# Performance work log

Measured on AMD Instinct MI355X. Metric: run time of the kernel, lower is better.

## Reference

```python
import jax, jax.numpy as jnp
import numpy as np

T, B, S, D = 512, 32, 512, 512
EPS = 1e-6  # LayerNorm eps


def _ln(x, g, b):
    m = jnp.mean(x, axis=-1, keepdims=True)
    v = jnp.mean((x - m) ** 2, axis=-1, keepdims=True)
    return g * (x - m) * jax.lax.rsqrt(v + EPS) + b


def setup_inputs() -> dict:
    key = jax.random.key(0)
    ks = jax.random.split(key, 10)
    sc = 1.0 / np.sqrt(D).astype(np.float32)
    return {
        "prev_layer": jax.random.normal(ks[0], (T, B, D), jnp.float32),
        "hidden": jax.random.normal(ks[1], (B, D), jnp.float32),
        "enc_output": jax.random.normal(ks[2], (B, S, D), jnp.float32),
        "memory_length": jax.random.randint(ks[3], (B,), 1, S + 1),
        # nn.Linear weights stored as [in, out] (transposed torch layout)
        "W_in": jax.random.normal(ks[4], (D, 3 * D), jnp.float32) * sc,
        "W_enc": jax.random.normal(ks[5], (D, D), jnp.float32) * sc,
        "W_attn_in": jax.random.normal(ks[6], (D, D), jnp.float32) * sc,
        "W_hidden": jax.random.normal(ks[7], (D, D), jnp.float32) * sc,
        "W_ctx": jax.random.normal(ks[8], (D, D), jnp.float32) * sc,
        # LayerNorm gains/biases (5 LNs)
        "g_pre": jnp.ones((3 * D,), jnp.float32), "b_pre": jnp.zeros((3 * D,), jnp.float32),
        "g_enc": jnp.ones((D,), jnp.float32), "b_enc": jnp.zeros((D,), jnp.float32),
        "g_attn": jnp.ones((D,), jnp.float32), "b_attn": jnp.zeros((D,), jnp.float32),
        "g_h": jnp.ones((D,), jnp.float32), "b_h": jnp.zeros((D,), jnp.float32),
        "g_c": jnp.ones((D,), jnp.float32), "b_c": jnp.zeros((D,), jnp.float32),
    }


def reference(prev_layer, hidden, enc_output, W_in, W_enc, W_attn_in, W_hidden,
              W_ctx, g_pre, b_pre, g_enc, b_enc, g_attn, b_attn, g_h, b_h,
              g_c, b_c, memory_length):
    d = prev_layer.shape[-1]
    sqrt_d = jnp.sqrt(jnp.asarray(d, prev_layer.dtype))
    # dropout is identity in eval mode
    preact = _ln(prev_layer @ W_in, g_pre, b_pre)          # [T,B,3D]
    pctx = _ln(enc_output @ W_enc, g_enc, b_enc)           # [B,S,D]
    z, h_gate, pl_t = jnp.split(preact, 3, axis=-1)
    z = jax.nn.sigmoid(z)
    h_gate = jax.nn.sigmoid(h_gate)

    # SRU-style linear recurrence: s_t = (1-z_t)*s_{t-1} + z_t*pl_t
    def step(h, zp):
        z_t, p_t = zp
        s = (1.0 - z_t) * h + z_t * p_t
        return s, s

    hidden_last, ss = jax.lax.scan(step, hidden, (z, pl_t))  # ss: [T,B,D]

    attn_in = _ln(ss @ W_attn_in, g_attn, b_attn)            # [T,B,D]
    align = jnp.einsum('tbd,bsd->bts', attn_in, pctx)        # [B,T,S]
    mask = jnp.arange(pctx.shape[1])[None, :] < memory_length[:, None]  # [B,S]
    align = jnp.where(mask[:, None, :], align, -jnp.inf)
    av = jax.nn.softmax(align / sqrt_d, axis=-1)             # [B,T,S]
    c = jnp.einsum('bts,bsd->tbd', av, pctx)                 # [T,B,D]
    attn_out = c / sqrt_d

    trans = _ln(ss @ W_hidden, g_h, b_h) + _ln(attn_out @ W_ctx, g_c, b_c)
    out = jnp.tanh(trans)
    out = (1.0 - h_gate) * out + h_gate * prev_layer         # [T,B,D]
    p_attn = jnp.transpose(av, (1, 0, 2))                    # [T,B,S]
    return out, hidden_last, p_attn
```

## Files before the change

### kernel.cpp

```cpp
#include <hip/hip_runtime.h>
#include <hip/hip_bf16.h>
#include <cmath>

#define T_ 512
#define B_ 32
#define S_ 512
#define D_ 512
#define D3_ 1536
#define NCH 16
#define CT (T_ / NCH)
static constexpr float LN_EPS = 1e-6f;
static constexpr float RSQRT_D = 0.044194173824159216f;

typedef __attribute__((ext_vector_type(8))) __bf16 bf16x8;
typedef __attribute__((ext_vector_type(4))) float f32x4;

struct __align__(8) bfx4 { __hip_bfloat16 x, y, z, w; };
struct __align__(16) u16x8 { unsigned short h[8]; };

__device__ __forceinline__ void g2l16(const void* g, void* l) {
    __builtin_amdgcn_global_load_lds(
        (const __attribute__((address_space(1))) unsigned int*)g,
        (__attribute__((address_space(3))) unsigned int*)l, 16, 0, 0);
}

__device__ __forceinline__ float xr_sum16(float v) {
    v += __shfl_xor(v, 1); v += __shfl_xor(v, 2);
    v += __shfl_xor(v, 4); v += __shfl_xor(v, 8); return v;
}
__device__ __forceinline__ float xr_max16(float v) {
    v = fmaxf(v, __shfl_xor(v, 1)); v = fmaxf(v, __shfl_xor(v, 2));
    v = fmaxf(v, __shfl_xor(v, 4)); v = fmaxf(v, __shfl_xor(v, 8)); return v;
}

__device__ __forceinline__ float sigmoidf_(float x) {
    return 1.f / (1.f + __expf(-x));
}
__device__ __forceinline__ float sigmoid_fast(float x) {
    return __fdividef(1.f, 1.f + __expf(-x));
}
__device__ __forceinline__ float tanh_fast(float x) {
    return 1.f - __fdividef(2.f, __expf(2.f * x) + 1.f);
}
__device__ __forceinline__ float bfu(unsigned short u) {
    unsigned int v = ((unsigned int)u) << 16;
    return __uint_as_float(v);
}

__global__ __launch_bounds__(256) void gemm_pre(
    const __hip_bfloat16* __restrict__ A,
    const __hip_bfloat16* __restrict__ Bw,
    __hip_bfloat16* __restrict__ preb,
    float2* __restrict__ part)
{
    __shared__ char smem[32768];

    const int lin = blockIdx.y * 12 + blockIdx.x;
    const int swz = (lin & 7) * 192 + (lin >> 3);
    const int bx = swz % 12, by = swz / 12;
    const int m0 = by * 128, n0 = bx * 128;
    const int tid = threadIdx.x, lane = tid & 63, w = tid >> 6;
    const int wm = (w >> 1) * 64, wn = (w & 1) * 64;
    const int srow = lane >> 2, skB = (lane & 3) * 16;
    const int q = lane >> 4, c = lane & 15;

    f32x4 acc[4][4];
#pragma unroll
    for (int i = 0; i < 4; i++)
#pragma unroll
        for (int j = 0; j < 4; j++) acc[i][j] = (f32x4)(0.0f);

    const char* ga0 = (const char*)(A + (long)(m0 + w * 16 + srow) * 512) + skB;
    const char* ga1 = (const char*)(A + (long)(m0 + (w + 4) * 16 + srow) * 512) + skB;
    const char* gb0 = (const char*)(Bw + (long)(n0 + w * 16 + srow) * 512) + skB;
    const char* gb1 = (const char*)(Bw + (long)(n0 + (w + 4) * 16 + srow) * 512) + skB;
    char* la0 = smem + w * 1024 + lane * 16;
    char* la1 = smem + (w + 4) * 1024 + lane * 16;
    char* lb0 = smem + 8192 + w * 1024 + lane * 16;
    char* lb1 = smem + 8192 + (w + 4) * 1024 + lane * 16;
    const char* Ar = smem + (wm + c) * 64 + q * 16;
    const char* Br = smem + 8192 + (wn + c) * 64 + q * 16;

    g2l16(ga0, la0);
    g2l16(ga1, la1);
    g2l16(gb0, lb0);
    g2l16(gb1, lb1);
    __syncthreads();

#pragma unroll
    for (int kk = 0; kk < 16; kk++) {
        const int cb = (kk & 1) << 14;
        const int nb = cb ^ 16384;
        if (kk < 15) {
            const long kb = (long)(kk + 1) * 64;
            g2l16(ga0 + kb, la0 + nb);
            g2l16(ga1 + kb, la1 + nb);
            g2l16(gb0 + kb, lb0 + nb);
            g2l16(gb1 + kb, lb1 + nb);
        }
        bf16x8 af[4], bfr[4];
#pragma unroll
        for (int i = 0; i < 4; i++) {
            af[i] = *(const bf16x8*)(Ar + cb + i * 1024);
            bfr[i] = *(const bf16x8*)(Br + cb + i * 1024);
        }
#pragma unroll
        for (int i = 0; i < 4; i++)
#pragma unroll
            for (int j = 0; j < 4; j++)
                acc[i][j] = __builtin_amdgcn_mfma_f32_16x16x32_bf16(
                    af[i], bfr[j], acc[i][j], 0, 0, 0);
        __syncthreads();
    }

    float2* sred = (float2*)smem;
#pragma unroll
    for (int i = 0; i < 4; i++)
#pragma unroll
        for (int r = 0; r < 4; r++) {
            float s = 0.f, qq = 0.f;
#pragma unroll
            for (int j = 0; j < 4; j++) {
                float v = acc[i][j][r]; s += v; qq += v * v;
            }
            s = xr_sum16(s); qq = xr_sum16(qq);
            if (c == 0) sred[(wm + i * 16 + q * 4 + r) * 2 + (w & 1)] =
                make_float2(s, qq);
        }
    __syncthreads();
    if ((w & 1) == 0 && c == 0) {
#pragma unroll
        for (int i = 0; i < 4; i++)
#pragma unroll
            for (int r = 0; r < 4; r++) {
                int row = wm + i * 16 + q * 4 + r;
                float2 a = sred[row * 2], b2 = sred[row * 2 + 1];
                part[(long)bx * 16384 + m0 + row] =
                    make_float2(a.x + b2.x, a.y + b2.y);
            }
    }
    __syncthreads();

    for (int p = 0; p < 2; p++) {
        if ((w >> 1) == p) {
#pragma unroll
            for (int i = 0; i < 4; i++)
#pragma unroll
                for (int j = 0; j < 4; j++)
#pragma unroll
                    for (int r = 0; r < 4; r++) {
                        int row = i * 16 + q * 4 + r;
                        int col = wn + j * 16 + c;
                        ((__hip_bfloat16*)smem)[row * 128 + col] =
                            __float2bfloat16(acc[i][j][r]);
                    }
        }
        __syncthreads();
#pragma unroll
        for (int rnd = 0; rnd < 4; rnd++) {
            int row = rnd * 16 + (tid >> 4);
            int ch = tid & 15;
            uint4 v = *(const uint4*)(smem + row * 256 + ch * 16);
            long grow = m0 + p * 64 + row;
            *(uint4*)((char*)preb + grow * 3072 + (long)n0 * 2 + ch * 16) = v;
        }
        __syncthreads();
    }
}

__global__ __launch_bounds__(256) void g128(
    const __hip_bfloat16* __restrict__ A, long ldaE,
    const __hip_bfloat16* __restrict__ Bw, long bStrideZ,
    __hip_bfloat16* __restrict__ out, long outStrideB,
    float2* __restrict__ part, float scale, int swizzle)
{
    __shared__ char smem[32768];
    int bx, by;
    if (gridDim.z > 1) {
        bx = blockIdx.x; by = blockIdx.y;
        A += (long)blockIdx.z * 512;
        Bw += (long)blockIdx.z * bStrideZ;
        out += (long)blockIdx.z * 512;
    } else if (swizzle) {
        const int nwg = gridDim.x * gridDim.y;
        const int lin = blockIdx.y * gridDim.x + blockIdx.x;
        const int cpx = nwg >> 3;
        const int swz = (lin & 7) * cpx + (lin >> 3);
        bx = swz % gridDim.x; by = swz / gridDim.x;
    } else { bx = blockIdx.x; by = blockIdx.y; }

    const int m0 = by * 128, n0 = bx * 128;
    const int tid = threadIdx.x, lane = tid & 63, w = tid >> 6;
    const int wm = (w >> 1) * 64, wn = (w & 1) * 64;
    const int srow = lane >> 2, skB = (lane & 3) * 16;
    const int q = lane >> 4, c = lane & 15;

    f32x4 acc[4][4];
#pragma unroll
    for (int i = 0; i < 4; i++)
#pragma unroll
        for (int j = 0; j < 4; j++) acc[i][j] = (f32x4)(0.0f);

    const char* ga0 = (const char*)(A + (long)(m0 + w * 16 + srow) * ldaE) + skB;
    const char* ga1 = (const char*)(A + (long)(m0 + (w + 4) * 16 + srow) * ldaE) + skB;
    const char* gb0 = (const char*)(Bw + (long)(n0 + w * 16 + srow) * 512) + skB;
    const char* gb1 = (const char*)(Bw + (long)(n0 + (w + 4) * 16 + srow) * 512) + skB;
    char* la0 = smem + w * 1024 + lane * 16;
    char* la1 = smem + (w + 4) * 1024 + lane * 16;
    char* lb0 = smem + 8192 + w * 1024 + lane * 16;
    char* lb1 = smem + 8192 + (w + 4) * 1024 + lane * 16;
    const char* Ar = smem + (wm + c) * 64 + q * 16;
    const char* Br = smem + 8192 + (wn + c) * 64 + q * 16;

    g2l16(ga0, la0);
    g2l16(ga1, la1);
    g2l16(gb0, lb0);
    g2l16(gb1, lb1);
    __syncthreads();

#pragma unroll
    for (int kk = 0; kk < 16; kk++) {
        const int cb = (kk & 1) << 14;
        const int nb = cb ^ 16384;
        if (kk < 15) {
            const long kb = (long)(kk + 1) * 64;
            g2l16(ga0 + kb, la0 + nb);
            g2l16(ga1 + kb, la1 + nb);
            g2l16(gb0 + kb, lb0 + nb);
            g2l16(gb1 + kb, lb1 + nb);
        }
        bf16x8 af[4], bfr[4];
#pragma unroll
        for (int i = 0; i < 4; i++) {
            af[i] = *(const bf16x8*)(Ar + cb + i * 1024);
            bfr[i] = *(const bf16x8*)(Br + cb + i * 1024);
        }
#pragma unroll
        for (int i = 0; i < 4; i++)
#pragma unroll
            for (int j = 0; j < 4; j++)
                acc[i][j] = __builtin_amdgcn_mfma_f32_16x16x32_bf16(
                    af[i], bfr[j], acc[i][j], 0, 0, 0);
        __syncthreads();
    }

    if (part) {
        float2* sred = (float2*)smem;
#pragma unroll
        for (int i = 0; i < 4; i++)
#pragma unroll
            for (int r = 0; r < 4; r++) {
                float s = 0.f, qq = 0.f;
#pragma unroll
                for (int j = 0; j < 4; j++) {
                    float v = acc[i][j][r]; s += v; qq += v * v;
                }
                s = xr_sum16(s); qq = xr_sum16(qq);
                if (c == 0) sred[(wm + i * 16 + q * 4 + r) * 2 + (w & 1)] =
                    make_float2(s, qq);
            }
        __syncthreads();
        if ((w & 1) == 0 && c == 0) {
#pragma unroll
            for (int i = 0; i < 4; i++)
#pragma unroll
                for (int r = 0; r < 4; r++) {
                    int row = wm + i * 16 + q * 4 + r;
                    float2 a = sred[row * 2], b2 = sred[row * 2 + 1];
                    part[(long)bx * 16384 + m0 + row] =
                        make_float2(a.x + b2.x, a.y + b2.y);
                }
        }
        __syncthreads();
    }

    for (int p = 0; p < 2; p++) {
        if ((w >> 1) == p) {
#pragma unroll
            for (int i = 0; i < 4; i++)
#pragma unroll
                for (int j = 0; j < 4; j++)
#pragma unroll
                    for (int r = 0; r < 4; r++) {
                        int row = i * 16 + q * 4 + r;
                        int col = wn + j * 16 + c;
                        ((__hip_bfloat16*)smem)[row * 128 + col] =
                            __float2bfloat16(acc[i][j][r] * scale);
                    }
        }
        __syncthreads();
#pragma unroll
        for (int rnd = 0; rnd < 4; rnd++) {
            int row = rnd * 16 + (tid >> 4);
            int ch = tid & 15;
            uint4 v = *(const uint4*)(smem + row * 256 + ch * 16);
            long grow = m0 + p * 64 + row;
            *(uint4*)((char*)out + grow * outStrideB + (long)n0 * 2 + ch * 16) = v;
        }
        __syncthreads();
    }
}

#define RC_BUF 34816
__device__ __forceinline__ void rows_core32_lds(
    const __hip_bfloat16* A, long lda,
    const __hip_bfloat16* B, long ldb,
    char* smem, f32x4 (&acc)[2][8])
{
    const int tid = threadIdx.x, lane = tid & 63, w = tid >> 6;
#pragma unroll
    for (int m = 0; m < 2; m++)
#pragma unroll
        for (int j = 0; j < 8; j++) acc[m][j] = (f32x4)(0.0f);

    const char* ga = (const char*)(A + (long)(w * 16 + (lane >> 2)) * lda) + (lane & 3) * 16;
    char* la = smem + w * 1024 + lane * 16;
    const char* gb = (const char*)(B + (long)(w * 128 + (lane >> 2)) * ldb) + (lane & 3) * 16;
    char* lb = smem + 2048 + w * 8192 + lane * 16;
    const long ldbB16 = (long)ldb * 32;
    const char* Ar = smem + (lane & 15) * 64 + (lane >> 4) * 16;
    const char* Br = smem + 2048 + (w * 128 + (lane & 15)) * 64 + (lane >> 4) * 16;

    if (w < 2) g2l16(ga, la);
#pragma unroll
    for (int s = 0; s < 8; s++) g2l16(gb + s * ldbB16, lb + s * 1024);
    __syncthreads();

#pragma unroll
    for (int kk = 0; kk < 16; kk++) {
        const int cb = (kk & 1) * RC_BUF;
        const int nb = ((kk & 1) ^ 1) * RC_BUF;
        if (kk < 15) {
            const long kb = (long)(kk + 1) * 64;
            if (w < 2) g2l16(ga + kb, la + nb);
#pragma unroll
            for (int s = 0; s < 8; s++)
                g2l16(gb + kb + s * ldbB16, lb + nb + s * 1024);
        }
        bf16x8 af[2], bfr[8];
#pragma unroll
        for (int m = 0; m < 2; m++) af[m] = *(const bf16x8*)(Ar + cb + m * 1024);
#pragma unroll
        for (int j = 0; j < 8; j++) bfr[j] = *(const bf16x8*)(Br + cb + j * 1024);
#pragma unroll
        for (int m = 0; m < 2; m++)
#pragma unroll
            for (int j = 0; j < 8; j++)
                acc[m][j] = __builtin_amdgcn_mfma_f32_16x16x32_bf16(
                    af[m], bfr[j], acc[m][j], 0, 0, 0);
        __syncthreads();
    }
}

__global__ __launch_bounds__(256, 2) void gemm_attn(
    const __hip_bfloat16* __restrict__ attninb,
    const __hip_bfloat16* __restrict__ pctxb,
    const int* __restrict__ mlen,
    float* __restrict__ pattn, __hip_bfloat16* __restrict__ pattnb)
{
    __shared__ char smem[69632];
    const int b = blockIdx.z;
    const long t0 = (long)blockIdx.y * 32;
    f32x4 acc[2][8];
    rows_core32_lds(attninb + (long)b * 512 + t0 * 16384, 16384,
                    pctxb + (long)b * 262144, 512, smem, acc);

    const int tid = threadIdx.x, lane = tid & 63, w = tid >> 6;
    const int q = lane >> 4, c = lane & 15;
    const int len = mlen[b];
    float* sred = (float*)smem;

#pragma unroll
    for (int m = 0; m < 2; m++)
#pragma unroll
        for (int r = 0; r < 4; r++) {
            float mx = -INFINITY;
#pragma unroll
            for (int j = 0; j < 8; j++) {
                int col = w * 128 + j * 16 + c;
                float v = acc[m][j][r] * RSQRT_D;
                acc[m][j][r] = v;
                if (col < len) mx = fmaxf(mx, v);
            }
            mx = xr_max16(mx);
            if (c == 0) sred[(m * 16 + q * 4 + r) * 4 + w] = mx;
        }
    __syncthreads();
    float rmax[2][4];
#pragma unroll
    for (int m = 0; m < 2; m++)
#pragma unroll
        for (int r = 0; r < 4; r++) {
            int row = m * 16 + q * 4 + r;
            rmax[m][r] = fmaxf(fmaxf(sred[row * 4], sred[row * 4 + 1]),
                               fmaxf(sred[row * 4 + 2], sred[row * 4 + 3]));
        }
    __syncthreads();
#pragma unroll
    for (int m = 0; m < 2; m++)
#pragma unroll
        for (int r = 0; r < 4; r++) {
            float s = 0.f;
#pragma unroll
            for (int j = 0; j < 8; j++) {
                int col = w * 128 + j * 16 + c;
                float e = (col < len) ? __expf(acc[m][j][r] - rmax[m][r]) : 0.f;
                acc[m][j][r] = e; s += e;
            }
            s = xr_sum16(s);
            if (c == 0) sred[(m * 16 + q * 4 + r) * 4 + w] = s;
        }
    __syncthreads();
    float rinv[2][4];
#pragma unroll
    for (int m = 0; m < 2; m++)
#pragma unroll
        for (int r = 0; r < 4; r++) {
            int row = m * 16 + q * 4 + r;
            rinv[m][r] = 1.f / (sred[row * 4] + sred[row * 4 + 1] +
                                sred[row * 4 + 2] + sred[row * 4 + 3]);
        }
    __syncthreads();

#pragma unroll
    for (int m = 0; m < 2; m++)
#pragma unroll
        for (int j = 0; j < 8; j++)
#pragma unroll
            for (int r = 0; r < 4; r++) {
                int row = m * 16 + q * 4 + r;
                int col = w * 128 + j * 16 + c;
                float p = acc[m][j][r] * rinv[m][r];
                acc[m][j][r] = p;
                pattn[((t0 + row) * 32 + b) * 512 + col] = p;
                ((__hip_bfloat16*)smem)[row * 512 + col] = __float2bfloat16(p);
            }
    __syncthreads();
#pragma unroll
    for (int rnd = 0; rnd < 8; rnd++) {
        int row = rnd * 4 + w;
        uint4 v = *(const uint4*)(smem + row * 1024 + lane * 16);
        *(uint4*)((char*)pattnb + ((t0 + row) * 32 + b) * 1024 + lane * 16) = v;
    }
}

__global__ __launch_bounds__(256) void stats4(
    const float2* __restrict__ part, float2* __restrict__ st)
{
    int r = blockIdx.x * 256 + threadIdx.x;
    float s = 0.f, qq = 0.f;
#pragma unroll
    for (int cb = 0; cb < 4; cb++) {
        float2 v = part[(long)cb * 16384 + r]; s += v.x; qq += v.y;
    }
    float m = s * (1.f / 512);
    float rs = rsqrtf(qq * (1.f / 512) - m * m + LN_EPS);
    st[r] = make_float2(m, rs);
}

__global__ __launch_bounds__(256) void ln_apply(
    __hip_bfloat16* __restrict__ x, const float2* __restrict__ st,
    const float* __restrict__ g, const float* __restrict__ bb)
{
    int i = blockIdx.x * 256 + threadIdx.x;
    int row = i >> 6;
    int c0 = (i & 63) * 8;
    float2 s = st[row];
    u16x8 v = *(const u16x8*)((const char*)x + (long)i * 16);
    float4 g0 = *(const float4*)(g + c0), g1 = *(const float4*)(g + c0 + 4);
    float4 b0 = *(const float4*)(bb + c0), b1 = *(const float4*)(bb + c0 + 4);
    float gv[8] = {g0.x, g0.y, g0.z, g0.w, g1.x, g1.y, g1.z, g1.w};
    float bv[8] = {b0.x, b0.y, b0.z, b0.w, b1.x, b1.y, b1.z, b1.w};
#pragma unroll
    for (int k = 0; k < 8; k++) {
        float f = (bfu(v.h[k]) - s.x) * s.y * gv[k] + bv[k];
        v.h[k] = __hip_bfloat16_raw(__float2bfloat16(f)).x;
    }
    *(u16x8*)((char*)x + (long)i * 16) = v;
}

__global__ __launch_bounds__(256) void fin_ep(
    const __hip_bfloat16* __restrict__ h2r, const __hip_bfloat16* __restrict__ h1r,
    const __hip_bfloat16* __restrict__ preb,
    const float2* __restrict__ st_c, const float2* __restrict__ st_h,
    const float2* __restrict__ st_p,
    const float* __restrict__ g_c, const float* __restrict__ b_c,
    const float* __restrict__ g_h, const float* __restrict__ b_h,
    const float* __restrict__ g_pre, const float* __restrict__ b_pre,
    const float* __restrict__ prev, float* __restrict__ out)
{
    const long m0 = (long)blockIdx.x * 32;
    const int tid = threadIdx.x;
#pragma unroll
    for (int ch = 0; ch < 16; ch++) {
        int f4 = ch * 256 + tid;
        int row = f4 >> 7;
        long rowg = m0 + row;
        int col = (f4 & 127) * 4;
        ushort4 h2 = *(const ushort4*)((const char*)h2r + rowg * 1024 + col * 2);
        ushort4 h1 = *(const ushort4*)((const char*)h1r + rowg * 1024 + col * 2);
        ushort4 hr = *(const ushort4*)((const char*)preb + rowg * 3072 + 1024 + col * 2);
        float4 pv = *(const float4*)(prev + rowg * 512 + col);
        float4 gc = *(const float4*)(g_c + col), bc = *(const float4*)(b_c + col);
        float4 gh = *(const float4*)(g_h + col), bh = *(const float4*)(b_h + col);
        float4 gp = *(const float4*)(g_pre + 512 + col);
        float4 bp = *(const float4*)(b_pre + 512 + col);
        float2 sc = st_c[rowg], sh = st_h[rowg], sp = st_p[rowg];
        auto fuse = [&](unsigned short h2u, unsigned short h1u, unsigned short hru,
                        float pvv, float gcv, float bcv, float ghv, float bhv,
                        float gpv, float bpv) -> float {
            float t2 = (bfu(h2u) - sc.x) * sc.y * gcv + bcv;
            float t1 = (bfu(h1u) - sh.x) * sh.y * ghv + bhv;
            float hg = sigmoid_fast((bfu(hru) - sp.x) * sp.y * gpv + bpv);
            return (1.f - hg) * tanh_fast(t1 + t2) + hg * pvv;
        };
        float4 o;
        o.x = fuse(h2.x, h1.x, hr.x, pv.x, gc.x, bc.x, gh.x, bh.x, gp.x, bp.x);
        o.y = fuse(h2.y, h1.y, hr.y, pv.y, gc.y, bc.y, gh.y, bh.y, gp.y, bp.y);
        o.z = fuse(h2.z, h1.z, hr.z, pv.z, gc.z, bc.z, gh.z, bh.z, gp.z, bp.z);
        o.w = fuse(h2.w, h1.w, hr.w, pv.w, gc.w, bc.w, gh.w, bh.w, gp.w, bp.w);
        *(float4*)(out + rowg * 512 + col) = o;
    }
}

__global__ __launch_bounds__(256) void cvt4(
    const float* __restrict__ x, __hip_bfloat16* __restrict__ y, int n4)
{
    int i = blockIdx.x * 256 + threadIdx.x;
    if (i >= n4) return;
    float4 v = ((const float4*)x)[i];
    bfx4 o;
    o.x = __float2bfloat16(v.x); o.y = __float2bfloat16(v.y);
    o.z = __float2bfloat16(v.z); o.w = __float2bfloat16(v.w);
    ((bfx4*)y)[i] = o;
}

__global__ __launch_bounds__(256) void wtrans(
    const float* __restrict__ w0, const float* __restrict__ w1,
    const float* __restrict__ w2, const float* __restrict__ w3,
    const float* __restrict__ w4, __hip_bfloat16* __restrict__ WT)
{
    int z = blockIdx.z;
    const float* W; long off; int N;
    if (z == 0)      { W = w0; off = 0;                N = 1536; }
    else if (z == 1) { W = w1; off = 786432;           N = 512; }
    else if (z == 2) { W = w2; off = 786432 + 262144;  N = 512; }
    else if (z == 3) { W = w3; off = 786432 + 524288;  N = 512; }
    else             { W = w4; off = 786432 + 786432;  N = 512; }
    int n0 = blockIdx.x * 32, k0 = blockIdx.y * 32;
    if (n0 >= N) return;
    __shared__ float t[32][33];
    int tx = threadIdx.x & 31, ty = threadIdx.x >> 5;
#pragma unroll
    for (int i = 0; i < 4; i++)
        t[ty + i * 8][tx] = W[(long)(k0 + ty + i * 8) * N + n0 + tx];
    __syncthreads();
    __hip_bfloat16* O = WT + off;
#pragma unroll
    for (int i = 0; i < 4; i++)
        O[(long)(n0 + ty + i * 8) * 512 + k0 + tx] =
            __float2bfloat16(t[tx][ty + i * 8]);
}

__global__ __launch_bounds__(256) void ptrans(
    const __hip_bfloat16* __restrict__ src, __hip_bfloat16* __restrict__ dst)
{
    long boff = (long)blockIdx.z * (S_ * D_);
    int d0 = blockIdx.x * 32, s0 = blockIdx.y * 32;
    __shared__ __hip_bfloat16 t[32][34];
    int tx = threadIdx.x & 31, ty = threadIdx.x >> 5;
#pragma unroll
    for (int i = 0; i < 4; i++)
        t[ty + i * 8][tx] = src[boff + (long)(s0 + ty + i * 8) * D_ + d0 + tx];
    __syncthreads();
#pragma unroll
    for (int i = 0; i < 4; i++)
        dst[boff + (long)(d0 + ty + i * 8) * S_ + s0 + tx] = t[tx][ty + i * 8];
}

__global__ __launch_bounds__(256) void stats_fin(
    const float2* __restrict__ part, float2* __restrict__ stats)
{
    int r = blockIdx.x * 256 + threadIdx.x;
    float s = 0.f, qq = 0.f;
#pragma unroll
    for (int cb = 0; cb < 12; cb++) {
        float2 v = part[(long)cb * 16384 + r]; s += v.x; qq += v.y;
    }
    float m = s * (1.f / 1536);
    float rs = rsqrtf(qq * (1.f / 1536) - m * m + LN_EPS);
    stats[r] = make_float2(m, rs);
}

__global__ __launch_bounds__(256) void scan_part1(
    const __hip_bfloat16* __restrict__ preb, const float2* __restrict__ stats,
    const float* __restrict__ gpre, const float* __restrict__ bpre,
    float* __restrict__ Ap, float* __restrict__ Bp)
{
    int idx = blockIdx.x * 256 + threadIdx.x;
    int b = idx >> 9, d = idx & 511;
    int ch = blockIdx.y;
    float gz = gpre[d], bz = bpre[d];
    float gp = gpre[1024 + d], bpv = bpre[1024 + d];
    float A = 1.f, s = 0.f;
    for (int t = ch * CT; t < (ch + 1) * CT; t++) {
        long row = (long)t * 32 + b;
        float2 st = stats[row];
        float zr = __bfloat162float(preb[row * 1536 + d]);
        float pr = __bfloat162float(preb[row * 1536 + 1024 + d]);
        float z = sigmoidf_((zr - st.x) * st.y * gz + bz);
        float pl = (pr - st.x) * st.y * gp + bpv;
        float a = 1.f - z;
        A *= a;
        s = a * s + z * pl;
    }
    Ap[ch * 16384 + idx] = A;
    Bp[ch * 16384 + idx] = s;
}

__global__ __launch_bounds__(256) void scan_part2(
    const float* __restrict__ Ap, const float* __restrict__ Bp,
    const float* __restrict__ h0, float* __restrict__ sin_,
    float* __restrict__ hlast)
{
    int idx = blockIdx.x * 256 + threadIdx.x;
    float s = h0[idx];
    for (int ch = 0; ch < NCH; ch++) {
        sin_[ch * 16384 + idx] = s;
        s = Ap[ch * 16384 + idx] * s + Bp[ch * 16384 + idx];
    }
    hlast[idx] = s;
}

__global__ __launch_bounds__(256) void scan_part3(
    const __hip_bfloat16* __restrict__ preb, const float2* __restrict__ stats,
    const float* __restrict__ gpre, const float* __restrict__ bpre,
    const float* __restrict__ sin_, __hip_bfloat16* __restrict__ ssb)
{
    int idx = blockIdx.x * 256 + threadIdx.x;
    int b = idx >> 9, d = idx & 511;
    int ch = blockIdx.y;
    float gz = gpre[d], bz = bpre[d];
    float gp = gpre[1024 + d], bpv = bpre[1024 + d];
    float s = sin_[ch * 16384 + idx];
    for (int t = ch * CT; t < (ch + 1) * CT; t++) {
        long row = (long)t * 32 + b;
        float2 st = stats[row];
        float zr = __bfloat162float(preb[row * 1536 + d]);
        float pr = __bfloat162float(preb[row * 1536 + 1024 + d]);
        float z = sigmoidf_((zr - st.x) * st.y * gz + bz);
        float pl = (pr - st.x) * st.y * gp + bpv;
        s += z * (pl - s);
        ssb[(long)t * 16384 + idx] = __float2bfloat16(s);
    }
}

extern "C" void kernel_launch(void* const* d_in, const int* in_sizes, int n_in,
                              void* d_out, int out_size, void* d_ws, size_t ws_size,
                              hipStream_t stream) {
    const float* prev  = (const float*)d_in[0];
    const float* hid0  = (const float*)d_in[1];
    const float* enc   = (const float*)d_in[2];
    const int*   mlen  = (const int*)  d_in[3];
    const float* W_in  = (const float*)d_in[4];
    const float* W_enc = (const float*)d_in[5];
    const float* W_att = (const float*)d_in[6];
    const float* W_hid = (const float*)d_in[7];
    const float* W_ctx = (const float*)d_in[8];
    const float* g_pre = (const float*)d_in[9];
    const float* b_pre = (const float*)d_in[10];
    const float* g_enc = (const float*)d_in[11];
    const float* b_enc = (const float*)d_in[12];
    const float* g_att = (const float*)d_in[13];
    const float* b_att = (const float*)d_in[14];
    const float* g_h   = (const float*)d_in[15];
    const float* b_h   = (const float*)d_in[16];
    const float* g_c   = (const float*)d_in[17];
    const float* b_c   = (const float*)d_in[18];

    float* out   = (float*)d_out;
    float* hlast = out + (long)T_ * B_ * D_;
    float* pattn = hlast + (long)B_ * D_;

    char* ws = (char*)d_ws;
    __hip_bfloat16* preb    = (__hip_bfloat16*)(ws);
    __hip_bfloat16* WT      = (__hip_bfloat16*)(ws + 50331648);
    __hip_bfloat16* prevb   = (__hip_bfloat16*)(ws + 54525952);
    __hip_bfloat16* encb    = (__hip_bfloat16*)(ws + 71303168);
    __hip_bfloat16* pctxb   = (__hip_bfloat16*)(ws + 88080384);
    __hip_bfloat16* pctxT   = (__hip_bfloat16*)(ws + 104857600);
    __hip_bfloat16* ssb     = (__hip_bfloat16*)(ws + 121634816);
    __hip_bfloat16* attninb = (__hip_bfloat16*)(ws + 138412032);
    __hip_bfloat16* pattnb  = (__hip_bfloat16*)(ws + 155189248);
    __hip_bfloat16* attnoutb= (__hip_bfloat16*)(ws + 171966464);
    __hip_bfloat16* h1n     = (__hip_bfloat16*)(ws + 188743680);
    float2* part            = (float2*)(ws + 205520896);
    float2* stats           = (float2*)(ws + 207093760);
    float* scanA            = (float*)(ws + 207224832);
    float* scanB            = (float*)(ws + 208273408);
    float* sinb             = (float*)(ws + 209321984);
    float2* stats_enc       = (float2*)(ws + 210370560);
    float2* stats_att       = (float2*)(ws + 210501632);
    float2* stats_h         = (float2*)(ws + 210632704);
    float2* stats_c         = (float2*)(ws + 210763776);

    __hip_bfloat16* h2raw = pattnb;

    const __hip_bfloat16* W_encT = WT + 786432;
    const __hip_bfloat16* W_attT = WT + 786432 + 262144;
    const __hip_bfloat16* W_hidT = WT + 786432 + 524288;
    const __hip_bfloat16* W_ctxT = WT + 786432 + 786432;

    dim3 blk(256);

    cvt4<<<8192, blk, 0, stream>>>(prev, prevb, 2097152);
    cvt4<<<8192, blk, 0, stream>>>(enc, encb, 2097152);
    wtrans<<<dim3(48, 16, 5), blk, 0, stream>>>(W_in, W_enc, W_att, W_hid,
                                                W_ctx, WT);

    gemm_pre<<<dim3(12, 128), blk, 0, stream>>>(prevb, WT, preb, part);
    stats_fin<<<64, blk, 0, stream>>>(part, stats);

    scan_part1<<<dim3(64, NCH), blk, 0, stream>>>(preb, stats, g_pre, b_pre,
                                                  scanA, scanB);
    scan_part2<<<64, blk, 0, stream>>>(scanA, scanB, hid0, sinb, hlast);
    scan_part3<<<dim3(64, NCH), blk, 0, stream>>>(preb, stats, g_pre, b_pre,
                                                  sinb, ssb);

    g128<<<dim3(4, 128), blk, 0, stream>>>(encb, 512, W_encT, 0, pctxb, 1024,
                                           part, 1.f, 1);
    stats4<<<64, blk, 0, stream>>>(part, stats_enc);
    ln_apply<<<4096, blk, 0, stream>>>(pctxb, stats_enc, g_enc, b_enc);
    ptrans<<<dim3(16, 16, 32), blk, 0, stream>>>(pctxb, pctxT);

    g128<<<dim3(4, 128), blk, 0, stream>>>(ssb, 512, W_attT, 0, attninb, 1024,
                                           part, 1.f, 1);
    stats4<<<64, blk, 0, stream>>>(part, stats_att);
    ln_apply<<<4096, blk, 0, stream>>>(attninb, stats_att, g_att, b_att);

    gemm_attn<<<dim3(1, 16, 32), blk, 0, stream>>>(attninb, pctxb, mlen,
                                                   pattn, pattnb);

    g128<<<dim3(4, 4, 32), blk, 0, stream>>>(pattnb, 16384, pctxT, 262144,
                                             attnoutb, 32768, nullptr,
                                             RSQRT_D, 0);

    g128<<<dim3(4, 128), blk, 0, stream>>>(ssb, 512, W_hidT, 0, h1n, 1024,
                                           part, 1.f, 1);
    stats4<<<64, blk, 0, stream>>>(part, stats_h);

    g128<<<dim3(4, 128), blk, 0, stream>>>(attnoutb, 512, W_ctxT, 0, h2raw,
                                           1024, part, 1.f, 1);
    stats4<<<64, blk, 0, stream>>>(part, stats_c);

    fin_ep<<<512, blk, 0, stream>>>(h2raw, h1n, preb, stats_c, stats_h, stats,
                                    g_c, b_c, g_h, b_h, g_pre, b_pre, prev,
                                    out);
}
```

Measured before the change: 448.5 us.

## Merge attn/hidden projections into one GEMM, fuse LN with pctx transpose, vectorize scan

The two GEMMs that share ssb as input (W_attn_in and W_hidden) become one wider GEMM writing a combined [rows, 1024] buffer C2, relying on the adjacent layout of the transposed weights. The LN apply for pctx is fused into the transpose kernel, and the scan kernels now process two channels per thread with paired loads. This removes a launch plus a re-read of ssb and a separate pass over pctx, in exchange for strided accesses into the combined buffer and reliance on the partial-stats layout for the second half.

```diff
diff --git a/kernel.cpp b/kernel.cpp
--- a/kernel.cpp
+++ b/kernel.cpp
@@ -353,16 +353,16 @@
 }
 
 __global__ __launch_bounds__(256, 2) void gemm_attn(
-    const __hip_bfloat16* __restrict__ attninb,
+    const __hip_bfloat16* __restrict__ attninC2,
     const __hip_bfloat16* __restrict__ pctxb,
     const int* __restrict__ mlen,
-    float* __restrict__ pattn, __hip_bfloat16* __restrict__ pattnb)
+    float* __restrict__ pattn, __hip_bfloat16* __restrict__ softb)
 {
     __shared__ char smem[69632];
     const int b = blockIdx.z;
     const long t0 = (long)blockIdx.y * 32;
     f32x4 acc[2][8];
-    rows_core32_lds(attninb + (long)b * 512 + t0 * 16384, 16384,
+    rows_core32_lds(attninC2 + (long)b * 1024 + t0 * 32768, 32768,
                     pctxb + (long)b * 262144, 512, smem, acc);
 
     const int tid = threadIdx.x, lane = tid & 63, w = tid >> 6;
@@ -440,7 +440,7 @@
     for (int rnd = 0; rnd < 8; rnd++) {
         int row = rnd * 4 + w;
         uint4 v = *(const uint4*)(smem + row * 1024 + lane * 16);
-        *(uint4*)((char*)pattnb + ((t0 + row) * 32 + b) * 1024 + lane * 16) = v;
+        *(uint4*)((char*)softb + ((t0 + row) * 32 + b) * 1024 + lane * 16) = v;
     }
 }
 
@@ -458,15 +458,17 @@
     st[r] = make_float2(m, rs);
 }
 
-__global__ __launch_bounds__(256) void ln_apply(
-    __hip_bfloat16* __restrict__ x, const float2* __restrict__ st,
+__global__ __launch_bounds__(256) void ln_apply_s(
+    __hip_bfloat16* __restrict__ x,
+    const float2* __restrict__ st,
     const float* __restrict__ g, const float* __restrict__ bb)
 {
     int i = blockIdx.x * 256 + threadIdx.x;
     int row = i >> 6;
     int c0 = (i & 63) * 8;
     float2 s = st[row];
-    u16x8 v = *(const u16x8*)((const char*)x + (long)i * 16);
+    char* p = (char*)x + (long)row * 2048 + (long)(i & 63) * 16;
+    u16x8 v = *(const u16x8*)p;
     float4 g0 = *(const float4*)(g + c0), g1 = *(const float4*)(g + c0 + 4);
     float4 b0 = *(const float4*)(bb + c0), b1 = *(const float4*)(bb + c0 + 4);
     float gv[8] = {g0.x, g0.y, g0.z, g0.w, g1.x, g1.y, g1.z, g1.w};
@@ -476,11 +478,40 @@
         float f = (bfu(v.h[k]) - s.x) * s.y * gv[k] + bv[k];
         v.h[k] = __hip_bfloat16_raw(__float2bfloat16(f)).x;
     }
-    *(u16x8*)((char*)x + (long)i * 16) = v;
+    *(u16x8*)p = v;
+}
+
+__global__ __launch_bounds__(256) void lnt(
+    __hip_bfloat16* __restrict__ x,
+    __hip_bfloat16* __restrict__ xT,
+    const float2* __restrict__ st,
+    const float* __restrict__ g, const float* __restrict__ bb)
+{
+    long boff = (long)blockIdx.z * (S_ * D_);
+    int d0 = blockIdx.x * 32, s0 = blockIdx.y * 32;
+    __shared__ __hip_bfloat16 t[32][34];
+    int tx = threadIdx.x & 31, ty = threadIdx.x >> 5;
+    float gv = g[d0 + tx], bv = bb[d0 + tx];
+#pragma unroll
+    for (int i = 0; i < 4; i++) {
+        int srow = s0 + ty + i * 8;
+        long row = (long)blockIdx.z * S_ + srow;
+        float2 s = st[row];
+        float f = (bfu(__hip_bfloat16_raw(x[boff + (long)srow * D_ + d0 + tx]).x)
+                   - s.x) * s.y * gv + bv;
+        __hip_bfloat16 h = __float2bfloat16(f);
+        t[ty + i * 8][tx] = h;
+        x[boff + (long)srow * D_ + d0 + tx] = h;
+    }
+    __syncthreads();
+#pragma unroll
+    for (int i = 0; i < 4; i++)
+        xT[boff + (long)(d0 + ty + i * 8) * S_ + s0 + tx] = t[tx][ty + i * 8];
 }
 
 __global__ __launch_bounds__(256) void fin_ep(
-    const __hip_bfloat16* __restrict__ h2r, const __hip_bfloat16* __restrict__ h1r,
+    const __hip_bfloat16* __restrict__ h2r,
+    const __hip_bfloat16* __restrict__ C2,
     const __hip_bfloat16* __restrict__ preb,
     const float2* __restrict__ st_c, const float2* __restrict__ st_h,
     const float2* __restrict__ st_p,
@@ -498,7 +529,7 @@
         long rowg = m0 + row;
         int col = (f4 & 127) * 4;
         ushort4 h2 = *(const ushort4*)((const char*)h2r + rowg * 1024 + col * 2);
-        ushort4 h1 = *(const ushort4*)((const char*)h1r + rowg * 1024 + col * 2);
+        ushort4 h1 = *(const ushort4*)((const char*)C2 + rowg * 2048 + 1024 + col * 2);
         ushort4 hr = *(const ushort4*)((const char*)preb + rowg * 3072 + 1024 + col * 2);
         float4 pv = *(const float4*)(prev + rowg * 512 + col);
         float4 gc = *(const float4*)(g_c + col), bc = *(const float4*)(b_c + col);
@@ -562,22 +593,6 @@
             __float2bfloat16(t[tx][ty + i * 8]);
 }
 
-__global__ __launch_bounds__(256) void ptrans(
-    const __hip_bfloat16* __restrict__ src, __hip_bfloat16* __restrict__ dst)
-{
-    long boff = (long)blockIdx.z * (S_ * D_);
-    int d0 = blockIdx.x * 32, s0 = blockIdx.y * 32;
-    __shared__ __hip_bfloat16 t[32][34];
-    int tx = threadIdx.x & 31, ty = threadIdx.x >> 5;
-#pragma unroll
-    for (int i = 0; i < 4; i++)
-        t[ty + i * 8][tx] = src[boff + (long)(s0 + ty + i * 8) * D_ + d0 + tx];
-    __syncthreads();
-#pragma unroll
-    for (int i = 0; i < 4; i++)
-        dst[boff + (long)(d0 + ty + i * 8) * S_ + s0 + tx] = t[tx][ty + i * 8];
-}
-
 __global__ __launch_bounds__(256) void stats_fin(
     const float2* __restrict__ part, float2* __restrict__ stats)
 {
@@ -597,25 +612,28 @@
     const float* __restrict__ gpre, const float* __restrict__ bpre,
     float* __restrict__ Ap, float* __restrict__ Bp)
 {
-    int idx = blockIdx.x * 256 + threadIdx.x;
-    int b = idx >> 9, d = idx & 511;
+    int i2 = blockIdx.x * 256 + threadIdx.x;
+    int b = i2 >> 8, d = (i2 & 255) * 2;
+    int idx = b * 512 + d;
     int ch = blockIdx.y;
-    float gz = gpre[d], bz = bpre[d];
-    float gp = gpre[1024 + d], bpv = bpre[1024 + d];
-    float A = 1.f, s = 0.f;
+    float2 gz = *(const float2*)(gpre + d), bz = *(const float2*)(bpre + d);
+    float2 gp = *(const float2*)(gpre + 1024 + d);
+    float2 bp = *(const float2*)(bpre + 1024 + d);
+    float A0 = 1.f, s0 = 0.f, A1 = 1.f, s1 = 0.f;
     for (int t = ch * CT; t < (ch + 1) * CT; t++) {
         long row = (long)t * 32 + b;
         float2 st = stats[row];
-        float zr = __bfloat162float(preb[row * 1536 + d]);
-        float pr = __bfloat162float(preb[row * 1536 + 1024 + d]);
-        float z = sigmoidf_((zr - st.x) * st.y * gz + bz);
-        float pl = (pr - st.x) * st.y * gp + bpv;
-        float a = 1.f - z;
-        A *= a;
-        s = a * s + z * pl;
-    }
-    Ap[ch * 16384 + idx] = A;
-    Bp[ch * 16384 + idx] = s;
+        ushort2 zr = *(const ushort2*)(preb + row * 1536 + d);
+        ushort2 pr = *(const ushort2*)(preb + row * 1536 + 1024 + d);
+        float z0 = sigmoidf_((bfu(zr.x) - st.x) * st.y * gz.x + bz.x);
+        float z1 = sigmoidf_((bfu(zr.y) - st.x) * st.y * gz.y + bz.y);
+        float p0 = (bfu(pr.x) - st.x) * st.y * gp.x + bp.x;
+        float p1 = (bfu(pr.y) - st.x) * st.y * gp.y + bp.y;
+        A0 *= (1.f - z0); s0 = (1.f - z0) * s0 + z0 * p0;
+        A1 *= (1.f - z1); s1 = (1.f - z1) * s1 + z1 * p1;
+    }
+    *(float2*)(Ap + ch * 16384 + idx) = make_float2(A0, A1);
+    *(float2*)(Bp + ch * 16384 + idx) = make_float2(s0, s1);
 }
 
 __global__ __launch_bounds__(256) void scan_part2(
@@ -637,21 +655,30 @@
     const float* __restrict__ gpre, const float* __restrict__ bpre,
     const float* __restrict__ sin_, __hip_bfloat16* __restrict__ ssb)
 {
-    int idx = blockIdx.x * 256 + threadIdx.x;
-    int b = idx >> 9, d = idx & 511;
+    int i2 = blockIdx.x * 256 + threadIdx.x;
+    int b = i2 >> 8, d = (i2 & 255) * 2;
+    int idx = b * 512 + d;
     int ch = blockIdx.y;
-    float gz = gpre[d], bz = bpre[d];
-    float gp = gpre[1024 + d], bpv = bpre[1024 + d];
-    float s = sin_[ch * 16384 + idx];
+    float2 gz = *(const float2*)(gpre + d), bz = *(const float2*)(bpre + d);
+    float2 gp = *(const float2*)(gpre + 1024 + d);
+    float2 bp = *(const float2*)(bpre + 1024 + d);
+    float2 sv = *(const float2*)(sin_ + ch * 16384 + idx);
+    float s0 = sv.x, s1 = sv.y;
     for (int t = ch * CT; t < (ch + 1) * CT; t++) {
         long row = (long)t * 32 + b;
         float2 st = stats[row];
-        float zr = __bfloat162float(preb[row * 1536 + d]);
-        float pr = __bfloat162float(preb[row * 1536 + 1024 + d]);
-        float z = sigmoidf_((zr - st.x) * st.y * gz + bz);
-        float pl = (pr - st.x) * st.y * gp + bpv;
-        s += z * (pl - s);
-        ssb[(long)t * 16384 + idx] = __float2bfloat16(s);
+        ushort2 zr = *(const ushort2*)(preb + row * 1536 + d);
+        ushort2 pr = *(const ushort2*)(preb + row * 1536 + 1024 + d);
+        float z0 = sigmoidf_((bfu(zr.x) - st.x) * st.y * gz.x + bz.x);
+        float z1 = sigmoidf_((bfu(zr.y) - st.x) * st.y * gz.y + bz.y);
+        float p0 = (bfu(pr.x) - st.x) * st.y * gp.x + bp.x;
+        float p1 = (bfu(pr.y) - st.x) * st.y * gp.y + bp.y;
+        s0 += z0 * (p0 - s0);
+        s1 += z1 * (p1 - s1);
+        ushort2 o;
+        o.x = __hip_bfloat16_raw(__float2bfloat16(s0)).x;
+        o.y = __hip_bfloat16_raw(__float2bfloat16(s1)).x;
+        *(ushort2*)(ssb + (long)t * 16384 + idx) = o;
     }
 }
 
@@ -690,10 +717,9 @@
     __hip_bfloat16* pctxb   = (__hip_bfloat16*)(ws + 88080384);
     __hip_bfloat16* pctxT   = (__hip_bfloat16*)(ws + 104857600);
     __hip_bfloat16* ssb     = (__hip_bfloat16*)(ws + 121634816);
-    __hip_bfloat16* attninb = (__hip_bfloat16*)(ws + 138412032);
-    __hip_bfloat16* pattnb  = (__hip_bfloat16*)(ws + 155189248);
+    __hip_bfloat16* C2      = (__hip_bfloat16*)(ws + 138412032);
     __hip_bfloat16* attnoutb= (__hip_bfloat16*)(ws + 171966464);
-    __hip_bfloat16* h1n     = (__hip_bfloat16*)(ws + 188743680);
+    __hip_bfloat16* softb   = (__hip_bfloat16*)(ws + 188743680);
     float2* part            = (float2*)(ws + 205520896);
     float2* stats           = (float2*)(ws + 207093760);
     float* scanA            = (float*)(ws + 207224832);
@@ -704,11 +730,10 @@
     float2* stats_h         = (float2*)(ws + 210632704);
     float2* stats_c         = (float2*)(ws + 210763776);
 
-    __hip_bfloat16* h2raw = pattnb;
+    __hip_bfloat16* h2raw = softb;
 
     const __hip_bfloat16* W_encT = WT + 786432;
     const __hip_bfloat16* W_attT = WT + 786432 + 262144;
-    const __hip_bfloat16* W_hidT = WT + 786432 + 524288;
     const __hip_bfloat16* W_ctxT = WT + 786432 + 786432;
 
     dim3 blk(256);
@@ -721,39 +746,36 @@
     gemm_pre<<<dim3(12, 128), blk, 0, stream>>>(prevb, WT, preb, part);
     stats_fin<<<64, blk, 0, stream>>>(part, stats);
 
-    scan_part1<<<dim3(64, NCH), blk, 0, stream>>>(preb, stats, g_pre, b_pre,
+    scan_part1<<<dim3(32, NCH), blk, 0, stream>>>(preb, stats, g_pre, b_pre,
                                                   scanA, scanB);
     scan_part2<<<64, blk, 0, stream>>>(scanA, scanB, hid0, sinb, hlast);
-    scan_part3<<<dim3(64, NCH), blk, 0, stream>>>(preb, stats, g_pre, b_pre,
+    scan_part3<<<dim3(32, NCH), blk, 0, stream>>>(preb, stats, g_pre, b_pre,
                                                   sinb, ssb);
 
     g128<<<dim3(4, 128), blk, 0, stream>>>(encb, 512, W_encT, 0, pctxb, 1024,
                                            part, 1.f, 1);
     stats4<<<64, blk, 0, stream>>>(part, stats_enc);
-    ln_apply<<<4096, blk, 0, stream>>>(pctxb, stats_enc, g_enc, b_enc);
-    ptrans<<<dim3(16, 16, 32), blk, 0, stream>>>(pctxb, pctxT);
-
-    g128<<<dim3(4, 128), blk, 0, stream>>>(ssb, 512, W_attT, 0, attninb, 1024,
+    lnt<<<dim3(16, 16, 32), blk, 0, stream>>>(pctxb, pctxT, stats_enc,
+                                              g_enc, b_enc);
+
+    g128<<<dim3(8, 128), blk, 0, stream>>>(ssb, 512, W_attT, 0, C2, 2048,
                                            part, 1.f, 1);
     stats4<<<64, blk, 0, stream>>>(part, stats_att);
-    ln_apply<<<4096, blk, 0, stream>>>(attninb, stats_att, g_att, b_att);
-
-    gemm_attn<<<dim3(1, 16, 32), blk, 0, stream>>>(attninb, pctxb, mlen,
-                                                   pattn, pattnb);
-
-    g128<<<dim3(4, 4, 32), blk, 0, stream>>>(pattnb, 16384, pctxT, 262144,
+    stats4<<<64, blk, 0, stream>>>(part + 4 * 16384, stats_h);
+    ln_apply_s<<<4096, blk, 0, stream>>>(C2, stats_att, g_att, b_att);
+
+    gemm_attn<<<dim3(1, 16, 32), blk, 0, stream>>>(C2, pctxb, mlen,
+                                                   pattn, softb);
+
+    g128<<<dim3(4, 4, 32), blk, 0, stream>>>(softb, 16384, pctxT, 262144,
                                              attnoutb, 32768, nullptr,
                                              RSQRT_D, 0);
-
-    g128<<<dim3(4, 128), blk, 0, stream>>>(ssb, 512, W_hidT, 0, h1n, 1024,
-                                           part, 1.f, 1);
-    stats4<<<64, blk, 0, stream>>>(part, stats_h);
 
     g128<<<dim3(4, 128), blk, 0, stream>>>(attnoutb, 512, W_ctxT, 0, h2raw,
                                            1024, part, 1.f, 1);
     stats4<<<64, blk, 0, stream>>>(part, stats_c);
 
-    fin_ep<<<512, blk, 0, stream>>>(h2raw, h1n, preb, stats_c, stats_h, stats,
+    fin_ep<<<512, blk, 0, stream>>>(h2raw, C2, preb, stats_c, stats_h, stats,
                                     g_c, b_c, g_h, b_h, g_pre, b_pre, prev,
                                     out);
 }
```

After: 436.2 us. 1.03x faster.
